# Kernel tuning notes

Hardware: AMD Instinct MI355X
Metric: run time of the kernel (lower is better)

## Reference

```python
import jax, jax.numpy as jnp
import numpy as np

B = 128        # graph pairs per batch
NPG = 512      # nodes per graph (equal-size graphs -> dense batch is a reshape)
D = 64         # input feature dim
DEG = 16       # avg degree
FILTERS = [64, 32, 16]
RDIM = 10      # resize_dim
CCH = 8        # conv channels per similarity image
MLP = [32, 16, 8, 4, 1]


def _make_edges(rng, n_graphs, npg, deg):
    E = n_graphs * npg * deg
    off = np.repeat(np.arange(n_graphs, dtype=np.int64) * npg, npg * deg)
    src = rng.integers(0, npg, E) + off
    dst = rng.integers(0, npg, E) + off
    return jnp.asarray(np.stack([src, dst]), dtype=jnp.int32)


def setup_inputs() -> dict:
    key = jax.random.key(0)
    ks = jax.random.split(key, 40)
    rng = np.random.default_rng(0)
    N = B * NPG
    inp = {}
    inp['x_i'] = jax.random.normal(ks[0], (N, D), jnp.float32)
    inp['x_j'] = jax.random.normal(ks[1], (N, D), jnp.float32)
    # GCN weights
    dims = [D] + FILTERS
    k = 2
    for li in range(3):
        fi, fo = dims[li], dims[li + 1]
        inp[f'gcn_w{li}'] = jax.random.normal(ks[k], (fi, fo), jnp.float32) / np.sqrt(fi); k += 1
        inp[f'gcn_b{li}'] = jnp.zeros((fo,), jnp.float32)
    # Conv filters: one Conv2d(1->CCH, 3x3, SAME) per GNN layer, OIHW kernels
    for li in range(3):
        inp[f'conv_w{li}'] = jax.random.normal(ks[k], (CCH, 1, 3, 3), jnp.float32) / 3.0; k += 1
        inp[f'conv_b{li}'] = jnp.zeros((CCH,), jnp.float32)
    # MLP (Linear-ReLU stack) + scoring layer
    mdims = [3 * CCH * RDIM * RDIM] + MLP
    for li in range(len(MLP)):
        fi, fo = mdims[li], mdims[li + 1]
        inp[f'mlp_w{li}'] = jax.random.normal(ks[k], (fi, fo), jnp.float32) / np.sqrt(fi); k += 1
        inp[f'mlp_b{li}'] = jnp.zeros((fo,), jnp.float32)
    inp['score_w'] = jax.random.normal(ks[k], (1, 1), jnp.float32); k += 1
    inp['score_b'] = jnp.zeros((1,), jnp.float32)
    # Graph structure (int constants)
    inp['edge_index_i'] = _make_edges(rng, B, NPG, DEG)
    inp['edge_index_j'] = _make_edges(rng, B, NPG, DEG)
    batch = jnp.asarray(np.repeat(np.arange(B, dtype=np.int64), NPG), dtype=jnp.int32)
    inp['batch_i'] = batch
    inp['batch_j'] = batch
    return inp


def _gcn(x, ei, w, b):
    # PyG GCNConv: A_hat = D^-1/2 (A + I) D^-1/2 ; out = A_hat (x W) + b
    src, dst = ei[0], ei[1]
    n = x.shape[0]
    xw = x @ w
    deg = jax.ops.segment_sum(jnp.ones(ei.shape[1], xw.dtype), dst, num_segments=n) + 1.0
    inv = jax.lax.rsqrt(deg)
    msg = xw[src] * (inv[src] * inv[dst])[:, None]
    agg = jax.ops.segment_sum(msg, dst, num_segments=n)
    return agg + xw * (inv * inv)[:, None] + b


def _forward(x_i, x_j, gcn_w0, gcn_b0, gcn_w1, gcn_b1, gcn_w2, gcn_b2,
             conv_w0, conv_b0, conv_w1, conv_b1, conv_w2, conv_b2,
             mlp_w0, mlp_b0, mlp_w1, mlp_b1, mlp_w2, mlp_b2, mlp_w3, mlp_b3, mlp_w4, mlp_b4,
             score_w, score_b, edge_index_i, edge_index_j):
    gws = [(gcn_w0, gcn_b0), (gcn_w1, gcn_b1), (gcn_w2, gcn_b2)]
    cvs = [(conv_w0, conv_b0), (conv_w1, conv_b1), (conv_w2, conv_b2)]
    embs = []
    for li, (w, b) in enumerate(gws):
        x_i = _gcn(x_i, edge_index_i, w, b)
        x_j = _gcn(x_j, edge_index_j, w, b)
        if li != len(gws) - 1:  # activation + dropout (eval mode -> identity)
            x_i = jax.nn.relu(x_i)
            x_j = jax.nn.relu(x_j)
        h_i = x_i.reshape(B, NPG, -1)  # to_dense_batch (equal-size graphs)
        h_j = x_j.reshape(B, NPG, -1)
        sim = jnp.einsum('bnd,bmd->bnm', h_i, h_j)  # [B, NPG, NPG]
        simr = jax.image.resize(sim, (B, RDIM, RDIM), method='bilinear', antialias=False)
        cw, cb = cvs[li]
        y = jax.lax.conv_general_dilated(simr[:, None], cw, (1, 1), 'SAME')
        y = jax.nn.relu(y + cb[None, :, None, None])  # [B, CCH, RDIM, RDIM]
        embs.append(y.reshape(B, -1))
    feat = jnp.concatenate(embs, axis=1)  # [B, 3*CCH*RDIM*RDIM]
    for w, b in [(mlp_w0, mlp_b0), (mlp_w1, mlp_b1), (mlp_w2, mlp_b2), (mlp_w3, mlp_b3), (mlp_w4, mlp_b4)]:
        feat = jax.nn.relu(feat @ w + b)
    score = jax.nn.sigmoid(feat @ score_w + score_b)
    return score.reshape(-1)


def reference(x_i, x_j, gcn_w0, gcn_b0, gcn_w1, gcn_b1, gcn_w2, gcn_b2,
              conv_w0, conv_b0, conv_w1, conv_b1, conv_w2, conv_b2,
              mlp_w0, mlp_b0, mlp_w1, mlp_b1, mlp_w2, mlp_b2, mlp_w3, mlp_b3, mlp_w4, mlp_b4,
              score_w, score_b, edge_index_i, edge_index_j, batch_i, batch_j):
    # batch_i/batch_j are implicit in the block layout (equal-size graphs)
    return _forward(x_i, x_j, gcn_w0, gcn_b0, gcn_w1, gcn_b1, gcn_w2, gcn_b2,
                    conv_w0, conv_b0, conv_w1, conv_b1, conv_w2, conv_b2,
                    mlp_w0, mlp_b0, mlp_w1, mlp_b1, mlp_w2, mlp_b2, mlp_w3, mlp_b3, mlp_w4, mlp_b4,
                    score_w, score_b, edge_index_i, edge_index_j)
```

## Files before the change

### kernel.cpp

```cpp
#include <hip/hip_runtime.h>
#include <hip/hip_fp16.h>

typedef float fvec4 __attribute__((ext_vector_type(4)));
typedef int ivec4 __attribute__((ext_vector_type(4)));

#define NN 65536
#define EE 1048576
#define BB 128
#define NPG 512
#define EPG 8192

__device__ __forceinline__ int pkrtz(float a, float b) {
  union { __half2 h; int i; } u; u.h = __floats2half2_rn(a, b); return u.i;
}
__device__ __forceinline__ float2 up2(int v) {
  union { int i; __half2 h; } u; u.i = v; return __half22float2(u.h);
}
__device__ __forceinline__ __half2 h2(int v) {
  union { int i; __half2 h; } u; u.i = v; return u.h;
}

#define ACCP(SP, w) { \
  (SP)[0] = __hadd2((SP)[0], h2((w)[0])); \
  (SP)[1] = __hadd2((SP)[1], h2((w)[1])); \
  (SP)[2] = __hadd2((SP)[2], h2((w)[2])); \
  (SP)[3] = __hadd2((SP)[3], h2((w)[3])); }

__device__ __forceinline__ int slot_of(int node) {
  constexpr int srows[20] = {25, 26, 76, 77, 127, 128, 178, 179, 229, 230,
                             281, 282, 332, 333, 383, 384, 434, 435, 485, 486};
  int slot = -1;
#pragma unroll
  for (int i = 0; i < 20; ++i)
    if (node == srows[i]) slot = i;
  return slot;
}
__constant__ int c_srows[20] = {25, 26, 76, 77, 127, 128, 178, 179, 229, 230,
                                281, 282, 332, 333, 383, 384, 434, 435, 485, 486};

__global__ __launch_bounds__(512)
void kA(const float* __restrict__ x_i, const float* __restrict__ x_j,
        const float* __restrict__ gw0, const float* __restrict__ gb0,
        const float* __restrict__ gw1,
        const int* __restrict__ ei, const int* __restrict__ ej,
        unsigned short* __restrict__ sidsG, unsigned int* __restrict__ packG,
        float* __restrict__ hs0, unsigned int* __restrict__ y1G) {
  __shared__ ivec4 buf[NPG * 4];
  __shared__ unsigned short sids[EPG];
  __shared__ int wsum[8];
  unsigned short* const dsts = reinterpret_cast<unsigned short*>(buf);
  int* const cnt = reinterpret_cast<int*>(reinterpret_cast<char*>(buf) + 16384);
  int* const posb = reinterpret_cast<int*>(reinterpret_cast<char*>(buf) + 18432);

  const int bid = blockIdx.x;
  const int half = bid & 1;
  const int sg = bid >> 1;
  const int side = sg >> 7, g = sg & 127;
  const float* __restrict__ x = side ? x_j : x_i;
  const int* __restrict__ eidx = side ? ej : ei;
  const int v = threadIdx.x;
  const int base = g * NPG, ebase = g * EPG;

  cnt[v] = 0;
  __syncthreads();
  for (int k = v; k < EPG; k += 512) {
    int d = eidx[EE + ebase + k] - base;
    dsts[k] = (unsigned short)d;
    atomicAdd(&cnt[d], 1);
  }
  __syncthreads();

  const int count = cnt[v];
  int xa = count;
  const int lane = v & 63;
#pragma unroll
  for (int d = 1; d < 64; d <<= 1) {
    int y = __shfl_up(xa, d, 64);
    if (lane >= d) xa += y;
  }
  const int wid = v >> 6;
  if (lane == 63) wsum[wid] = xa;
  __syncthreads();
  if (v == 0) {
    int a = 0;
#pragma unroll
    for (int i = 0; i < 8; ++i) { int tv = wsum[i]; wsum[i] = a; a += tv; }
  }
  __syncthreads();
  const int start = xa - count + wsum[wid];
  posb[v] = start;
  if (half == 0) packG[sg * NPG + v] = ((unsigned int)start << 16) | (unsigned int)count;
  __syncthreads();

  for (int k = v; k < EPG; k += 512) {
    int lv = eidx[ebase + k] - base;
    int p = atomicAdd(&posb[dsts[k]], 1);
    sids[p] = (unsigned short)lv;
  }

  fvec4 a0[8];
#pragma unroll
  for (int q = 0; q < 8; ++q) a0[q] = fvec4{0.f, 0.f, 0.f, 0.f};
  {
    const fvec4* xv = reinterpret_cast<const fvec4*>(x + (size_t)(base + v) * 64);
    const float* w0h = gw0 + half * 32;
#pragma unroll 1
    for (int k16 = 0; k16 < 4; ++k16) {
      fvec4 xq[4];
#pragma unroll
      for (int u = 0; u < 4; ++u) xq[u] = xv[4 * k16 + u];
#pragma unroll
      for (int u = 0; u < 4; ++u) {
#pragma unroll
        for (int j = 0; j < 4; ++j) {
          const float xk = xq[u][j];
          const fvec4* wr = reinterpret_cast<const fvec4*>(w0h + (size_t)(16 * k16 + 4 * u + j) * 64);
#pragma unroll
          for (int q = 0; q < 8; ++q) a0[q] += xk * wr[q];
        }
      }
    }
  }
  __syncthreads();

  if (half == 0) {
    const int* srcI = reinterpret_cast<const int*>(sids);
    int* dstI = reinterpret_cast<int*>(sidsG + (size_t)sg * EPG);
    for (int k = v; k < EPG / 2; k += 512) dstI[k] = srcI[k];
  }

  const float inv_v = rsqrtf((float)count + 1.0f);
  const int myKey = (v << 2) | ((v >> 1) & 3);
  __half2 sp[16];
#pragma unroll
  for (int q_ = 0; q_ < 4; ++q_) {
    fvec4 m0 = a0[2 * q_] * inv_v;
    fvec4 m1 = a0[2 * q_ + 1] * inv_v;
    ivec4 w_;
    w_[0] = pkrtz(m0[0], m0[1]);
    w_[1] = pkrtz(m0[2], m0[3]);
    w_[2] = pkrtz(m1[0], m1[1]);
    w_[3] = pkrtz(m1[2], m1[3]);
    buf[myKey ^ q_] = w_;
    sp[4 * q_ + 0] = h2(w_[0]);
    sp[4 * q_ + 1] = h2(w_[1]);
    sp[4 * q_ + 2] = h2(w_[2]);
    sp[4 * q_ + 3] = h2(w_[3]);
  }
  __syncthreads();

  {
    int e = start;
    const int end = start + count;
    for (; e + 2 <= end; e += 2) {
      const int la = sids[e], lb = sids[e + 1];
      const int Ka = (la << 2) | ((la >> 1) & 3);
      const int Kb = (lb << 2) | ((lb >> 1) & 3);
      const ivec4 a0_ = buf[Ka], a1_ = buf[Ka ^ 1], a2_ = buf[Ka ^ 2], a3_ = buf[Ka ^ 3];
      const ivec4 b0_ = buf[Kb], b1_ = buf[Kb ^ 1], b2_ = buf[Kb ^ 2], b3_ = buf[Kb ^ 3];
      ACCP(sp + 0, a0_) ACCP(sp + 4, a1_) ACCP(sp + 8, a2_) ACCP(sp + 12, a3_)
      ACCP(sp + 0, b0_) ACCP(sp + 4, b1_) ACCP(sp + 8, b2_) ACCP(sp + 12, b3_)
    }
    if (e < end) {
      const int la = sids[e];
      const int Ka = (la << 2) | ((la >> 1) & 3);
      const ivec4 a0_ = buf[Ka], a1_ = buf[Ka ^ 1], a2_ = buf[Ka ^ 2], a3_ = buf[Ka ^ 3];
      ACCP(sp + 0, a0_) ACCP(sp + 4, a1_) ACCP(sp + 8, a2_) ACCP(sp + 12, a3_)
    }
  }

  fvec4 s[8];
#pragma unroll
  for (int q_ = 0; q_ < 4; ++q_) {
    float2 f0 = __half22float2(sp[4 * q_ + 0]);
    float2 f1 = __half22float2(sp[4 * q_ + 1]);
    float2 f2 = __half22float2(sp[4 * q_ + 2]);
    float2 f3 = __half22float2(sp[4 * q_ + 3]);
    s[2 * q_][0] = f0.x; s[2 * q_][1] = f0.y; s[2 * q_][2] = f1.x; s[2 * q_][3] = f1.y;
    s[2 * q_ + 1][0] = f2.x; s[2 * q_ + 1][1] = f2.y; s[2 * q_ + 1][2] = f3.x; s[2 * q_ + 1][3] = f3.y;
  }

  const int slot = slot_of(v);
  const int hb = (side * BB + g) * 20;
  fvec4 y1P[8];
#pragma unroll
  for (int p = 0; p < 8; ++p) y1P[p] = fvec4{0.f, 0.f, 0.f, 0.f};
  {
    const fvec4* gb0v = reinterpret_cast<const fvec4*>(gb0 + half * 32);
    fvec4* hp = reinterpret_cast<fvec4*>(hs0 + ((size_t)hb + slot) * 64 + half * 32);
#pragma unroll
    for (int q = 0; q < 8; ++q) {
      fvec4 o = s[q] * inv_v + gb0v[q];
#pragma unroll
      for (int j = 0; j < 4; ++j) o[j] = fmaxf(o[j], 0.f);
      if (slot >= 0) hp[q] = o;
#pragma unroll
      for (int j = 0; j < 4; ++j) {
        const float hf = o[j];
        const fvec4* wr = reinterpret_cast<const fvec4*>(gw1 + (size_t)(half * 32 + q * 4 + j) * 32);
#pragma unroll
        for (int p = 0; p < 8; ++p) y1P[p] += hf * wr[p];
      }
    }
  }
  {
    unsigned int* yp = y1G + ((size_t)(sg * 2 + half) * NPG + v) * 16;
#pragma unroll
    for (int w = 0; w < 16; ++w)
      yp[w] = (unsigned int)pkrtz(y1P[w >> 1][(w & 1) * 2], y1P[w >> 1][(w & 1) * 2 + 1]);
  }
}

__global__ __launch_bounds__(512)
void kB(const float* __restrict__ gb1, const float* __restrict__ gw2,
        const unsigned short* __restrict__ sidsG, const unsigned int* __restrict__ packG,
        const unsigned int* __restrict__ y1G,
        float* __restrict__ hs1, unsigned int* __restrict__ y2G) {
  __shared__ ivec4 buf[NPG * 2];
  __shared__ unsigned short sids[EPG];
  const int bid = blockIdx.x;
  const int half = bid & 1;
  const int sg = bid >> 1;
  const int side = sg >> 7, g = sg & 127;
  const int v = threadIdx.x;

  {
    const int* srcI = reinterpret_cast<const int*>(sidsG + (size_t)sg * EPG);
    int* dstI = reinterpret_cast<int*>(sids);
    for (int k = v; k < EPG / 2; k += 512) dstI[k] = srcI[k];
  }
  const unsigned int pack = packG[sg * NPG + v];
  const int count = (int)(pack & 0xffffu);
  const int nstart = (int)(pack >> 16);
  const float inv_v = rsqrtf((float)count + 1.0f);

  fvec4 s1[4];
  {
    const unsigned int* p0 = y1G + ((size_t)(sg * 2 + 0) * NPG + v) * 16 + half * 8;
    const unsigned int* p1 = y1G + ((size_t)(sg * 2 + 1) * NPG + v) * 16 + half * 8;
#pragma unroll
    for (int w = 0; w < 8; ++w) {
      float2 fa = up2((int)p0[w]);
      float2 fb = up2((int)p1[w]);
      s1[w >> 1][(w & 1) * 2] = (fa.x + fb.x) * inv_v;
      s1[w >> 1][(w & 1) * 2 + 1] = (fa.y + fb.y) * inv_v;
    }
  }
  const int myKey = (v << 1) | (v & 1);
  __half2 sp[8];
  {
    ivec4 w0, w1;
    w0[0] = pkrtz(s1[0][0], s1[0][1]); w0[1] = pkrtz(s1[0][2], s1[0][3]);
    w0[2] = pkrtz(s1[1][0], s1[1][1]); w0[3] = pkrtz(s1[1][2], s1[1][3]);
    w1[0] = pkrtz(s1[2][0], s1[2][1]); w1[1] = pkrtz(s1[2][2], s1[2][3]);
    w1[2] = pkrtz(s1[3][0], s1[3][1]); w1[3] = pkrtz(s1[3][2], s1[3][3]);
    buf[myKey] = w0;
    buf[myKey ^ 1] = w1;
    sp[0] = h2(w0[0]); sp[1] = h2(w0[1]); sp[2] = h2(w0[2]); sp[3] = h2(w0[3]);
    sp[4] = h2(w1[0]); sp[5] = h2(w1[1]); sp[6] = h2(w1[2]); sp[7] = h2(w1[3]);
  }
  __syncthreads();

  {
    int e = nstart;
    const int end = nstart + count;
    for (; e + 2 <= end; e += 2) {
      const int la = sids[e], lb = sids[e + 1];
      const int Ka = (la << 1) | (la & 1), Kb = (lb << 1) | (lb & 1);
      const ivec4 a0_ = buf[Ka], a1_ = buf[Ka ^ 1];
      const ivec4 b0_ = buf[Kb], b1_ = buf[Kb ^ 1];
      ACCP(sp + 0, a0_) ACCP(sp + 4, a1_)
      ACCP(sp + 0, b0_) ACCP(sp + 4, b1_)
    }
    if (e < end) {
      const int la = sids[e];
      const int Ka = (la << 1) | (la & 1);
      const ivec4 a0_ = buf[Ka], a1_ = buf[Ka ^ 1];
      ACCP(sp + 0, a0_) ACCP(sp + 4, a1_)
    }
  }
#pragma unroll
  for (int w = 0; w < 8; ++w) {
    float2 f = __half22float2(sp[w]);
    s1[w >> 1][(w & 1) * 2] = f.x;
    s1[w >> 1][(w & 1) * 2 + 1] = f.y;
  }

  const int slot = slot_of(v);
  const int hb = (side * BB + g) * 20;
  fvec4 y2P[4];
#pragma unroll
  for (int p = 0; p < 4; ++p) y2P[p] = fvec4{0.f, 0.f, 0.f, 0.f};
  {
    const fvec4* gb1v = reinterpret_cast<const fvec4*>(gb1 + half * 16);
    fvec4* hp = reinterpret_cast<fvec4*>(hs1 + ((size_t)hb + slot) * 32 + half * 16);
#pragma unroll
    for (int q = 0; q < 4; ++q) {
      fvec4 o = s1[q] * inv_v + gb1v[q];
#pragma unroll
      for (int j = 0; j < 4; ++j) o[j] = fmaxf(o[j], 0.f);
      if (slot >= 0) hp[q] = o;
#pragma unroll
      for (int j = 0; j < 4; ++j) {
        const float hf = o[j];
        const fvec4* wr = reinterpret_cast<const fvec4*>(gw2 + (size_t)(half * 16 + q * 4 + j) * 16);
#pragma unroll
        for (int p = 0; p < 4; ++p) y2P[p] += hf * wr[p];
      }
    }
  }
  {
    unsigned int* yp = y2G + ((size_t)(sg * 2 + half) * NPG + v) * 8;
#pragma unroll
    for (int w = 0; w < 8; ++w)
      yp[w] = (unsigned int)pkrtz(y2P[w >> 1][(w & 1) * 2], y2P[w >> 1][(w & 1) * 2 + 1]);
  }
}

__global__ __launch_bounds__(512)
void kC(const float* __restrict__ gb2,
        const unsigned short* __restrict__ sidsG, const unsigned int* __restrict__ packG,
        const unsigned int* __restrict__ y2G, float* __restrict__ hs2) {
  __shared__ ivec4 buf[NPG * 2];
  __shared__ unsigned short sids[EPG];
  const int sg = blockIdx.x;
  const int side = sg >> 7, g = sg & 127;
  const int v = threadIdx.x;

  {
    const int* srcI = reinterpret_cast<const int*>(sidsG + (size_t)sg * EPG);
    int* dstI = reinterpret_cast<int*>(sids);
    for (int k = v; k < EPG / 2; k += 512) dstI[k] = srcI[k];
  }
  const unsigned int pack = packG[sg * NPG + v];
  const int count = (int)(pack & 0xffffu);
  const float inv_v = rsqrtf((float)count + 1.0f);

  const int myKey = (v << 1) | (v & 1);
  {
    const unsigned int* p0 = y2G + ((size_t)(sg * 2 + 0) * NPG + v) * 8;
    const unsigned int* p1 = y2G + ((size_t)(sg * 2 + 1) * NPG + v) * 8;
    fvec4 y2[4];
#pragma unroll
    for (int w = 0; w < 8; ++w) {
      float2 fa = up2((int)p0[w]);
      float2 fb = up2((int)p1[w]);
      y2[w >> 1][(w & 1) * 2] = (fa.x + fb.x) * inv_v;
      y2[w >> 1][(w & 1) * 2 + 1] = (fa.y + fb.y) * inv_v;
    }
    ivec4 w0, w1;
    w0[0] = pkrtz(y2[0][0], y2[0][1]); w0[1] = pkrtz(y2[0][2], y2[0][3]);
    w0[2] = pkrtz(y2[1][0], y2[1][1]); w0[3] = pkrtz(y2[1][2], y2[1][3]);
    w1[0] = pkrtz(y2[2][0], y2[2][1]); w1[1] = pkrtz(y2[2][2], y2[2][3]);
    w1[2] = pkrtz(y2[3][0], y2[3][1]); w1[3] = pkrtz(y2[3][2], y2[3][3]);
    buf[myKey] = w0;
    buf[myKey ^ 1] = w1;
  }
  __syncthreads();

  if (v < 20) {
    const int n = c_srows[v];
    const unsigned int cp = packG[sg * NPG + n];
    const int ccount = (int)(cp & 0xffffu);
    const int cstart = (int)(cp >> 16);
    const float cinv = rsqrtf((float)ccount + 1.0f);
    const int ckey = (n << 1) | (n & 1);
    __half2 sp[8];
    {
      const ivec4 w0 = buf[ckey], w1 = buf[ckey ^ 1];
      sp[0] = h2(w0[0]); sp[1] = h2(w0[1]); sp[2] = h2(w0[2]); sp[3] = h2(w0[3]);
      sp[4] = h2(w1[0]); sp[5] = h2(w1[1]); sp[6] = h2(w1[2]); sp[7] = h2(w1[3]);
    }
    for (int e = cstart; e < cstart + ccount; ++e) {
      const int la = sids[e];
      const int Ka = (la << 1) | (la & 1);
      const ivec4 w0 = buf[Ka], w1 = buf[Ka ^ 1];
      ACCP(sp + 0, w0) ACCP(sp + 4, w1)
    }
    const int hb = (side * BB + g) * 20;
    const fvec4* gb2v = reinterpret_cast<const fvec4*>(gb2);
    fvec4* hp = reinterpret_cast<fvec4*>(hs2 + ((size_t)hb + v) * 16);
#pragma unroll
    for (int q = 0; q < 4; ++q) {
      float2 f0 = __half22float2(sp[2 * q]);
      float2 f1 = __half22float2(sp[2 * q + 1]);
      fvec4 s2;
      s2[0] = f0.x; s2[1] = f0.y; s2[2] = f1.x; s2[3] = f1.y;
      hp[q] = s2 * cinv + gb2v[q];
    }
  }
}

__global__ __launch_bounds__(256) void k_head(const float* __restrict__ hs0, const float* __restrict__ hs1,
                                              const float* __restrict__ hs2,
                                              const float* __restrict__ cw0, const float* __restrict__ cb0,
                                              const float* __restrict__ cw1, const float* __restrict__ cb1,
                                              const float* __restrict__ cw2, const float* __restrict__ cb2,
                                              const float* __restrict__ mw0, const float* __restrict__ mb0,
                                              const float* __restrict__ mw1, const float* __restrict__ mb1,
                                              const float* __restrict__ mw2, const float* __restrict__ mb2,
                                              const float* __restrict__ mw3, const float* __restrict__ mb3,
                                              const float* __restrict__ mw4, const float* __restrict__ mb4,
                                              const float* __restrict__ sw, const float* __restrict__ sb,
                                              float* __restrict__ out) {
  __shared__ float hi[2240];
  __shared__ float hj[2240];
  __shared__ float sim[400];
  __shared__ float simr[100];
  __shared__ float feat[2400];
  __shared__ float red[256];
  __shared__ float mbuf[60];
  const int b = blockIdx.x, t = threadIdx.x;

  for (int k = t; k < 1280; k += 256) {
    hi[k] = hs0[(size_t)(0 * BB + b) * 1280 + k];
    hj[k] = hs0[(size_t)(1 * BB + b) * 1280 + k];
  }
  for (int k = t; k < 640; k += 256) {
    hi[1280 + k] = hs1[(size_t)(0 * BB + b) * 640 + k];
    hj[1280 + k] = hs1[(size_t)(1 * BB + b) * 640 + k];
  }
  for (int k = t; k < 320; k += 256) {
    hi[1920 + k] = hs2[(size_t)(0 * BB + b) * 320 + k];
    hj[1920 + k] = hs2[(size_t)(1 * BB + b) * 320 + k];
  }
  __syncthreads();

  const int Fs[3] = {64, 32, 16};
  const int HOFF[3] = {0, 1280, 1920};
  const float* CW[3] = {cw0, cw1, cw2};
  const float* CB[3] = {cb0, cb1, cb2};

  for (int li = 0; li < 3; ++li) {
    const int F = Fs[li];
    const float* Hi = hi + HOFF[li];
    const float* Hj = hj + HOFF[li];
    for (int p = t; p < 400; p += 256) {
      int r = p / 20, cq = p % 20;
      float a = 0.0f;
      for (int d = 0; d < F; ++d) a += Hi[r * F + d] * Hj[cq * F + d];
      sim[p] = a;
    }
    __syncthreads();
    if (t < 100) {
      int oy = t / 10, ox = t % 10;
      float cy = (oy + 0.5f) * (512.0f / 10.0f) - 0.5f;
      float cx = (ox + 0.5f) * (512.0f / 10.0f) - 0.5f;
      float fy = cy - floorf(cy);
      float fx = cx - floorf(cx);
      int r0 = 2 * oy, c0 = 2 * ox;
      float s00 = sim[r0 * 20 + c0], s01 = sim[r0 * 20 + c0 + 1];
      float s10 = sim[(r0 + 1) * 20 + c0], s11 = sim[(r0 + 1) * 20 + c0 + 1];
      simr[t] = (1.0f - fy) * ((1.0f - fx) * s00 + fx * s01) + fy * ((1.0f - fx) * s10 + fx * s11);
    }
    __syncthreads();
    const float* cw = CW[li];
    const float* cb = CB[li];
    for (int idx = t; idx < 800; idx += 256) {
      int cch = idx / 100, rem = idx % 100, y = rem / 10, x = rem % 10;
      float a = cb[cch];
#pragma unroll
      for (int ky = 0; ky < 3; ++ky) {
#pragma unroll
        for (int kx = 0; kx < 3; ++kx) {
          int iy = y + ky - 1, ix = x + kx - 1;
          if (iy >= 0 && iy < 10 && ix >= 0 && ix < 10)
            a += cw[cch * 9 + ky * 3 + kx] * simr[iy * 10 + ix];
        }
      }
      feat[li * 800 + idx] = fmaxf(a, 0.0f);
    }
    __syncthreads();
  }

  {
    int f = t & 31, part = t >> 5;
    float a = 0.0f;
    int k0 = part * 300;
    for (int k = k0; k < k0 + 300; ++k) a += feat[k] * mw0[k * 32 + f];
    red[t] = a;
    __syncthreads();
    if (t < 32) {
      float s = mb0[t];
#pragma unroll
      for (int p = 0; p < 8; ++p) s += red[p * 32 + t];
      mbuf[t] = fmaxf(s, 0.0f);
    }
    __syncthreads();
  }
  if (t < 16) {
    float s = mb1[t];
    for (int k = 0; k < 32; ++k) s += mbuf[k] * mw1[k * 16 + t];
    mbuf[32 + t] = fmaxf(s, 0.0f);
  }
  __syncthreads();
  if (t < 8) {
    float s = mb2[t];
    for (int k = 0; k < 16; ++k) s += mbuf[32 + k] * mw2[k * 8 + t];
    mbuf[48 + t] = fmaxf(s, 0.0f);
  }
  __syncthreads();
  if (t < 4) {
    float s = mb3[t];
    for (int k = 0; k < 8; ++k) s += mbuf[48 + k] * mw3[k * 4 + t];
    mbuf[56 + t] = fmaxf(s, 0.0f);
  }
  __syncthreads();
  if (t == 0) {
    float s = mb4[0];
    for (int k = 0; k < 4; ++k) s += mbuf[56 + k] * mw4[k];
    s = fmaxf(s, 0.0f);
    float z = s * sw[0] + sb[0];
    out[b] = 1.0f / (1.0f + expf(-z));
  }
}

extern "C" void kernel_launch(void* const* d_in, const int* in_sizes, int n_in,
                              void* d_out, int out_size, void* d_ws, size_t ws_size,
                              hipStream_t stream) {
  (void)in_sizes; (void)n_in; (void)out_size; (void)ws_size;
  const float* x_i = (const float*)d_in[0];
  const float* x_j = (const float*)d_in[1];
  const float* gw0 = (const float*)d_in[2];
  const float* gb0 = (const float*)d_in[3];
  const float* gw1 = (const float*)d_in[4];
  const float* gb1 = (const float*)d_in[5];
  const float* gw2 = (const float*)d_in[6];
  const float* gb2 = (const float*)d_in[7];
  const float* cw0 = (const float*)d_in[8];
  const float* cb0 = (const float*)d_in[9];
  const float* cw1 = (const float*)d_in[10];
  const float* cb1 = (const float*)d_in[11];
  const float* cw2 = (const float*)d_in[12];
  const float* cb2 = (const float*)d_in[13];
  const float* mw0 = (const float*)d_in[14];
  const float* mb0 = (const float*)d_in[15];
  const float* mw1 = (const float*)d_in[16];
  const float* mb1 = (const float*)d_in[17];
  const float* mw2 = (const float*)d_in[18];
  const float* mb2 = (const float*)d_in[19];
  const float* mw3 = (const float*)d_in[20];
  const float* mb3 = (const float*)d_in[21];
  const float* mw4 = (const float*)d_in[22];
  const float* mb4 = (const float*)d_in[23];
  const float* scw = (const float*)d_in[24];
  const float* scb = (const float*)d_in[25];
  const int* ei = (const int*)d_in[26];
  const int* ej = (const int*)d_in[27];
  float* out = (float*)d_out;

  char* p = (char*)d_ws;
  auto take = [&](size_t bytes) {
    char* r = p;
    p += (bytes + 255) & ~(size_t)255;
    return r;
  };
  float* hs0 = (float*)take((size_t)2 * BB * 20 * 64 * 4);
  float* hs1 = (float*)take((size_t)2 * BB * 20 * 32 * 4);
  float* hs2 = (float*)take((size_t)2 * BB * 20 * 16 * 4);
  unsigned short* sidsG = (unsigned short*)take((size_t)2 * BB * EPG * 2);
  unsigned int* packG = (unsigned int*)take((size_t)2 * BB * NPG * 4);
  unsigned int* y1G = (unsigned int*)take((size_t)2 * BB * 2 * NPG * 16 * 4);
  unsigned int* y2G = (unsigned int*)take((size_t)2 * BB * 2 * NPG * 8 * 4);

  kA<<<2 * BB * 2, 512, 0, stream>>>(x_i, x_j, gw0, gb0, gw1, ei, ej,
                                     sidsG, packG, hs0, y1G);
  kB<<<2 * BB * 2, 512, 0, stream>>>(gb1, gw2, sidsG, packG, y1G, hs1, y2G);
  kC<<<2 * BB, 512, 0, stream>>>(gb2, sidsG, packG, y2G, hs2);
  k_head<<<BB, 256, 0, stream>>>(hs0, hs1, hs2, cw0, cb0, cw1, cb1, cw2, cb2,
                                 mw0, mb0, mw1, mb1, mw2, mb2, mw3, mb3, mw4, mb4,
                                 scw, scb, out);
}
```

Before: 119.2 us.

## Sort nodes by in-degree so wavefronts process similar-degree nodes together

Builds a per-graph counting sort of nodes by in-degree (capped at 63) in kA and remaps each thread to a degree-sorted node, storing the permutation for kB. Threads in the same wavefront then run aggregation loops of similar length, which is meant to reduce divergence and idle lanes in the gather loop. In exchange it adds an extra barrier, shared atomics, a small permutation array in global memory, and scattered (uncoalesced) reads of x and y1G and writes of y1G/y2G, since rows are now indexed by node instead of thread. kC is left unchanged.

```diff
diff --git a/kernel.cpp b/kernel.cpp
--- a/kernel.cpp
+++ b/kernel.cpp
@@ -44,13 +44,18 @@
         const float* __restrict__ gw1,
         const int* __restrict__ ei, const int* __restrict__ ej,
         unsigned short* __restrict__ sidsG, unsigned int* __restrict__ packG,
+        unsigned short* __restrict__ nodeOfG,
         float* __restrict__ hs0, unsigned int* __restrict__ y1G) {
   __shared__ ivec4 buf[NPG * 4];
   __shared__ unsigned short sids[EPG];
   __shared__ int wsum[8];
-  unsigned short* const dsts = reinterpret_cast<unsigned short*>(buf);
-  int* const cnt = reinterpret_cast<int*>(reinterpret_cast<char*>(buf) + 16384);
-  int* const posb = reinterpret_cast<int*>(reinterpret_cast<char*>(buf) + 18432);
+  char* const bufc = reinterpret_cast<char*>(buf);
+  unsigned short* const dsts = reinterpret_cast<unsigned short*>(bufc);
+  int* const cnt = reinterpret_cast<int*>(bufc + 16384);
+  int* const posb = reinterpret_cast<int*>(bufc + 18432);
+  int* const nodeOf = reinterpret_cast<int*>(bufc + 20480);
+  int* const bins = reinterpret_cast<int*>(bufc + 22528);
+  int* const binpos = reinterpret_cast<int*>(bufc + 22784);
 
   const int bid = blockIdx.x;
   const int half = bid & 1;
@@ -62,6 +67,7 @@
   const int base = g * NPG, ebase = g * EPG;
 
   cnt[v] = 0;
+  if (v < 64) bins[v] = 0;
   __syncthreads();
   for (int k = v; k < EPG; k += 512) {
     int d = eidx[EE + ebase + k] - base;
@@ -71,6 +77,8 @@
   __syncthreads();
 
   const int count = cnt[v];
+  const int deg = count > 63 ? 63 : count;
+  atomicAdd(&bins[deg], 1);
   int xa = count;
   const int lane = v & 63;
 #pragma unroll
@@ -81,15 +89,29 @@
   const int wid = v >> 6;
   if (lane == 63) wsum[wid] = xa;
   __syncthreads();
-  if (v == 0) {
-    int a = 0;
-#pragma unroll
-    for (int i = 0; i < 8; ++i) { int tv = wsum[i]; wsum[i] = a; a += tv; }
+  if (v < 64) {
+    if (v == 0) {
+      int a = 0;
+#pragma unroll
+      for (int i = 0; i < 8; ++i) { int tv = wsum[i]; wsum[i] = a; a += tv; }
+    }
+    int c = bins[v];
+    int xb = c;
+#pragma unroll
+    for (int d = 1; d < 64; d <<= 1) {
+      int y = __shfl_up(xb, d, 64);
+      if (v >= d) xb += y;
+    }
+    binpos[v] = xb - c;
   }
   __syncthreads();
   const int start = xa - count + wsum[wid];
   posb[v] = start;
   if (half == 0) packG[sg * NPG + v] = ((unsigned int)start << 16) | (unsigned int)count;
+  {
+    int rank = atomicAdd(&binpos[deg], 1);
+    nodeOf[rank] = v;
+  }
   __syncthreads();
 
   for (int k = v; k < EPG; k += 512) {
@@ -97,12 +119,18 @@
     int p = atomicAdd(&posb[dsts[k]], 1);
     sids[p] = (unsigned short)lv;
   }
+  __syncthreads();
+
+  const int node = nodeOf[v];
+  const int ncount = cnt[node];
+  const int nstart = posb[node] - ncount;
+  if (half == 0) nodeOfG[sg * NPG + v] = (unsigned short)node;
 
   fvec4 a0[8];
 #pragma unroll
   for (int q = 0; q < 8; ++q) a0[q] = fvec4{0.f, 0.f, 0.f, 0.f};
   {
-    const fvec4* xv = reinterpret_cast<const fvec4*>(x + (size_t)(base + v) * 64);
+    const fvec4* xv = reinterpret_cast<const fvec4*>(x + (size_t)(base + node) * 64);
     const float* w0h = gw0 + half * 32;
 #pragma unroll 1
     for (int k16 = 0; k16 < 4; ++k16) {
@@ -129,8 +157,8 @@
     for (int k = v; k < EPG / 2; k += 512) dstI[k] = srcI[k];
   }
 
-  const float inv_v = rsqrtf((float)count + 1.0f);
-  const int myKey = (v << 2) | ((v >> 1) & 3);
+  const float inv_v = rsqrtf((float)ncount + 1.0f);
+  const int myKey = (node << 2) | ((node >> 1) & 3);
   __half2 sp[16];
 #pragma unroll
   for (int q_ = 0; q_ < 4; ++q_) {
@@ -150,8 +178,8 @@
   __syncthreads();
 
   {
-    int e = start;
-    const int end = start + count;
+    int e = nstart;
+    const int end = nstart + ncount;
     for (; e + 2 <= end; e += 2) {
       const int la = sids[e], lb = sids[e + 1];
       const int Ka = (la << 2) | ((la >> 1) & 3);
@@ -180,7 +208,7 @@
     s[2 * q_ + 1][0] = f2.x; s[2 * q_ + 1][1] = f2.y; s[2 * q_ + 1][2] = f3.x; s[2 * q_ + 1][3] = f3.y;
   }
 
-  const int slot = slot_of(v);
+  const int slot = slot_of(node);
   const int hb = (side * BB + g) * 20;
   fvec4 y1P[8];
 #pragma unroll
@@ -204,7 +232,7 @@
     }
   }
   {
-    unsigned int* yp = y1G + ((size_t)(sg * 2 + half) * NPG + v) * 16;
+    unsigned int* yp = y1G + ((size_t)(sg * 2 + half) * NPG + node) * 16;
 #pragma unroll
     for (int w = 0; w < 16; ++w)
       yp[w] = (unsigned int)pkrtz(y1P[w >> 1][(w & 1) * 2], y1P[w >> 1][(w & 1) * 2 + 1]);
@@ -214,7 +242,7 @@
 __global__ __launch_bounds__(512)
 void kB(const float* __restrict__ gb1, const float* __restrict__ gw2,
         const unsigned short* __restrict__ sidsG, const unsigned int* __restrict__ packG,
-        const unsigned int* __restrict__ y1G,
+        const unsigned short* __restrict__ nodeOfG, const unsigned int* __restrict__ y1G,
         float* __restrict__ hs1, unsigned int* __restrict__ y2G) {
   __shared__ ivec4 buf[NPG * 2];
   __shared__ unsigned short sids[EPG];
@@ -229,15 +257,16 @@
     int* dstI = reinterpret_cast<int*>(sids);
     for (int k = v; k < EPG / 2; k += 512) dstI[k] = srcI[k];
   }
-  const unsigned int pack = packG[sg * NPG + v];
+  const int node = nodeOfG[sg * NPG + v];
+  const unsigned int pack = packG[sg * NPG + node];
   const int count = (int)(pack & 0xffffu);
   const int nstart = (int)(pack >> 16);
   const float inv_v = rsqrtf((float)count + 1.0f);
 
   fvec4 s1[4];
   {
-    const unsigned int* p0 = y1G + ((size_t)(sg * 2 + 0) * NPG + v) * 16 + half * 8;
-    const unsigned int* p1 = y1G + ((size_t)(sg * 2 + 1) * NPG + v) * 16 + half * 8;
+    const unsigned int* p0 = y1G + ((size_t)(sg * 2 + 0) * NPG + node) * 16 + half * 8;
+    const unsigned int* p1 = y1G + ((size_t)(sg * 2 + 1) * NPG + node) * 16 + half * 8;
 #pragma unroll
     for (int w = 0; w < 8; ++w) {
       float2 fa = up2((int)p0[w]);
@@ -246,7 +275,7 @@
       s1[w >> 1][(w & 1) * 2 + 1] = (fa.y + fb.y) * inv_v;
     }
   }
-  const int myKey = (v << 1) | (v & 1);
+  const int myKey = (node << 1) | (node & 1);
   __half2 sp[8];
   {
     ivec4 w0, w1;
@@ -286,7 +315,7 @@
     s1[w >> 1][(w & 1) * 2 + 1] = f.y;
   }
 
-  const int slot = slot_of(v);
+  const int slot = slot_of(node);
   const int hb = (side * BB + g) * 20;
   fvec4 y2P[4];
 #pragma unroll
@@ -310,7 +339,7 @@
     }
   }
   {
-    unsigned int* yp = y2G + ((size_t)(sg * 2 + half) * NPG + v) * 8;
+    unsigned int* yp = y2G + ((size_t)(sg * 2 + half) * NPG + node) * 8;
 #pragma unroll
     for (int w = 0; w < 8; ++w)
       yp[w] = (unsigned int)pkrtz(y2P[w >> 1][(w & 1) * 2], y2P[w >> 1][(w & 1) * 2 + 1]);
@@ -560,12 +589,13 @@
   float* hs2 = (float*)take((size_t)2 * BB * 20 * 16 * 4);
   unsigned short* sidsG = (unsigned short*)take((size_t)2 * BB * EPG * 2);
   unsigned int* packG = (unsigned int*)take((size_t)2 * BB * NPG * 4);
+  unsigned short* nodeOfG = (unsigned short*)take((size_t)2 * BB * NPG * 2);
   unsigned int* y1G = (unsigned int*)take((size_t)2 * BB * 2 * NPG * 16 * 4);
   unsigned int* y2G = (unsigned int*)take((size_t)2 * BB * 2 * NPG * 8 * 4);
 
   kA<<<2 * BB * 2, 512, 0, stream>>>(x_i, x_j, gw0, gb0, gw1, ei, ej,
-                                     sidsG, packG, hs0, y1G);
-  kB<<<2 * BB * 2, 512, 0, stream>>>(gb1, gw2, sidsG, packG, y1G, hs1, y2G);
+                                     sidsG, packG, nodeOfG, hs0, y1G);
+  kB<<<2 * BB * 2, 512, 0, stream>>>(gb1, gw2, sidsG, packG, nodeOfG, y1G, hs1, y2G);
   kC<<<2 * BB, 512, 0, stream>>>(gb2, sidsG, packG, y2G, hs2);
   k_head<<<BB, 256, 0, stream>>>(hs0, hs1, hs2, cw0, cb0, cw1, cb1, cw2, cb2,
                                  mw0, mb0, mw1, mb1, mw2, mb2, mw3, mb3, mw4, mb4,
```

Result: faster. 116.7 us (-2.2%).
